# Performance work log

Measured on AMD Instinct MI355X. Metric: run time of the kernel, lower is better.

Reference implementation:

```python
import jax, jax.numpy as jnp
import numpy as np

B, S, H, NH = 4, 384, 256, 8
DH = H // NH


def setup_inputs() -> dict:
    key = jax.random.key(0)
    ks = jax.random.split(key, 16)
    inp = {
        'key': jax.random.normal(ks[0], (B, S, H), jnp.float32),
        'query': jax.random.normal(ks[1], (B, S, H), jnp.float32),
        'value': jax.random.normal(ks[2], (B, S, H), jnp.float32),
        'rel_pos_embedding': jax.random.normal(ks[3], (B, S, S, H), jnp.float32),
        'seq_len': jax.random.randint(ks[4], (B,), 0, 300, jnp.int32),
        'lex_num': jax.random.randint(ks[5], (B,), 0, 84, jnp.int32),
        'Wk': jax.random.normal(ks[6], (H, H), jnp.float32) / np.sqrt(H),
        'bk': jnp.zeros((H,), jnp.float32),
        'Wq': jax.random.normal(ks[7], (H, H), jnp.float32) / np.sqrt(H),
        'bq': jnp.zeros((H,), jnp.float32),
        'Wv': jax.random.normal(ks[8], (H, H), jnp.float32) / np.sqrt(H),
        'bv': jnp.zeros((H,), jnp.float32),
        'Wr': jax.random.normal(ks[9], (H, H), jnp.float32) / np.sqrt(H),
        'br': jnp.zeros((H,), jnp.float32),
    }
    return inp


def reference(key, query, value, rel_pos_embedding, seq_len, lex_num,
              Wk, bk, Wq, bq, Wv, bv, Wr, br):
    b, s, h = key.shape
    # linear projections then split heads: [B, NH, S, DH]
    k = (key @ Wk + bk).reshape(b, s, NH, DH).transpose(0, 2, 1, 3)
    q = (query @ Wq + bq).reshape(b, s, NH, DH).transpose(0, 2, 1, 3)
    v = (value @ Wv + bv).reshape(b, s, NH, DH).transpose(0, 2, 1, 3)
    # relative position projection: [B, Sq, Sk, NH, DH]
    rel = (rel_pos_embedding @ Wr + br).reshape(b, s, s, NH, DH)
    # content term A_C: [B, NH, Sq, Sk]
    A_C = jnp.einsum('bhqd,bhkd->bhqk', q, k)
    # relative term B_D: query dotted with per-(q,k)-pair rel embedding
    B_D = jnp.einsum('bhqd,bqkhd->bhqk', q, rel)
    # key mask from seq_len + lex_num (no scaling by sqrt(d), per original)
    valid = jnp.arange(s)[None, :] < (seq_len + lex_num)[:, None]  # [B, Sk]
    score = jnp.where(valid[:, None, None, :], A_C + B_D, jnp.float32(-1e15))
    attn = jax.nn.softmax(score, axis=-1)
    out = jnp.einsum('bhqk,bhkd->bhqd', attn, v)
    # merge heads: [B, S, H]; note: original does NOT apply w_final
    return out.transpose(0, 2, 1, 3).reshape(b, s, h)
```

## Files before the change

### kernel.cpp

```cpp
#include <hip/hip_runtime.h>
#include <hip/hip_bf16.h>

#define S_  384
#define H_  256
#define NH_ 8
#define DH_ 32
#define B_  4
#define PADK 385

typedef _Float16 f16x8 __attribute__((ext_vector_type(8)));
typedef _Float16 f16x4 __attribute__((ext_vector_type(4)));
typedef float    f32x4 __attribute__((ext_vector_type(4)));

__global__ __launch_bounds__(256) void proj_kernel(
    const float* __restrict__ query, const float* __restrict__ key, const float* __restrict__ value,
    const float* __restrict__ Wq, const float* __restrict__ bq,
    const float* __restrict__ Wk, const float* __restrict__ bk,
    const float* __restrict__ Wv, const float* __restrict__ bv,
    float* __restrict__ Qb, _Float16* __restrict__ Kf, float* __restrict__ Vb)
{
    __shared__ __align__(16) float As[32][36];
    __shared__ __align__(16) float Bs[32][68];
    const int t = threadIdx.x;
    const int m0g = blockIdx.x * 32;
    const int n0g = blockIdx.y * 64;
    const int z = blockIdx.z;
    const float* X    = (z == 0) ? query : (z == 1 ? key : value);
    const float* W    = (z == 0) ? Wq    : (z == 1 ? Wk  : Wv);
    const float* bias = (z == 0) ? bq    : (z == 1 ? bk  : bv);

    const int tn = (t & 15) * 4;
    const int tm = (t >> 4) * 2;
    float acc0[4] = {0.f,0.f,0.f,0.f};
    float acc1[4] = {0.f,0.f,0.f,0.f};

    const int ar = t >> 3, ac4 = (t & 7) * 4;
    const int brr = t >> 4, bc4 = (t & 15) * 4;

    for (int kt = 0; kt < 8; ++kt) {
        const int k0 = kt * 32;
        float4 av  = *(const float4*)&X[(size_t)(m0g + ar) * H_ + k0 + ac4];
        float4 bv0 = *(const float4*)&W[(size_t)(k0 + brr)      * H_ + n0g + bc4];
        float4 bv1 = *(const float4*)&W[(size_t)(k0 + brr + 16) * H_ + n0g + bc4];
        *(float4*)&As[ar][ac4] = av;
        *(float4*)&Bs[brr][bc4] = bv0;
        *(float4*)&Bs[brr + 16][bc4] = bv1;
        __syncthreads();
        #pragma unroll
        for (int c = 0; c < 32; ++c) {
            const float a0 = As[tm][c], a1 = As[tm + 1][c];
            const float4 b4 = *(const float4*)&Bs[c][tn];
            acc0[0] += a0 * b4.x; acc0[1] += a0 * b4.y; acc0[2] += a0 * b4.z; acc0[3] += a0 * b4.w;
            acc1[0] += a1 * b4.x; acc1[1] += a1 * b4.y; acc1[2] += a1 * b4.z; acc1[3] += a1 * b4.w;
        }
        __syncthreads();
    }
    const float4 bi = *(const float4*)&bias[n0g + tn];
    float4 o0 = make_float4(acc0[0] + bi.x, acc0[1] + bi.y, acc0[2] + bi.z, acc0[3] + bi.w);
    float4 o1 = make_float4(acc1[0] + bi.x, acc1[1] + bi.y, acc1[2] + bi.z, acc1[3] + bi.w);
    if (z == 1) {
        f16x4 h0 = { (_Float16)o0.x, (_Float16)o0.y, (_Float16)o0.z, (_Float16)o0.w };
        f16x4 h1 = { (_Float16)o1.x, (_Float16)o1.y, (_Float16)o1.z, (_Float16)o1.w };
        *(f16x4*)&Kf[(size_t)(m0g + tm)     * H_ + n0g + tn] = h0;
        *(f16x4*)&Kf[(size_t)(m0g + tm + 1) * H_ + n0g + tn] = h1;
    } else {
        float* Out = (z == 0) ? Qb : Vb;
        *(float4*)&Out[(size_t)(m0g + tm)     * H_ + n0g + tn] = o0;
        *(float4*)&Out[(size_t)(m0g + tm + 1) * H_ + n0g + tn] = o1;
    }
}

__global__ __launch_bounds__(256) void qw_kernel(
    const float* __restrict__ Qb, const float* __restrict__ Wr,
    _Float16* __restrict__ Af)
{
    __shared__ __align__(16) float Qs[16][36];
    const int t = threadIdx.x;
    const int m0 = blockIdx.x * 16;
    const int h = blockIdx.y;

    float4 wr4[8];
    #pragma unroll
    for (int j = 0; j < 8; ++j)
        wr4[j] = *(const float4*)&Wr[(size_t)t * H_ + h * DH_ + j * 4];

    if (t < 128) {
        const int r = t >> 3, d4 = (t & 7) * 4;
        *(float4*)&Qs[r][d4] = *(const float4*)&Qb[(size_t)(m0 + r) * H_ + h * DH_ + d4];
    }
    __syncthreads();

    const bool own = ((t >> 5) == h);
    #pragma unroll 4
    for (int r = 0; r < 16; ++r) {
        float acc = 0.f;
        #pragma unroll
        for (int j = 0; j < 8; ++j) {
            const float4 qv = *(const float4*)&Qs[r][j * 4];
            acc += qv.x * wr4[j].x + qv.y * wr4[j].y + qv.z * wr4[j].z + qv.w * wr4[j].w;
        }
        _Float16* arow = Af + ((size_t)(m0 + r) * NH_ + h) * 512;
        arow[t] = (_Float16)acc;
        arow[256 + t] = own ? (_Float16)Qs[r][t & 31] : (_Float16)0.0f;
    }
}

__global__ __launch_bounds__(256) void attn_kernel(
    const float* __restrict__ rpe, const _Float16* __restrict__ Af,
    const _Float16* __restrict__ Kf, const float* __restrict__ Vb,
    const int* __restrict__ seq_len, const int* __restrict__ lex_num,
    float* __restrict__ out)
{
    __shared__ float sc[NH_ * PADK];
    __shared__ __align__(16) _Float16 stg[4][16][256];
    const int blk = blockIdx.x;
    const int b = blk / S_;
    const int q = blk - b * S_;
    const int t = threadIdx.x;
    const int lane = t & 63;
    const int wave = t >> 6;
    int limit = seq_len[b] + lex_num[b];
    limit = limit < 0 ? 0 : (limit > S_ ? S_ : limit);
    const size_t rowQ = (size_t)(b * S_ + q);

    if (limit == 0) {
        float acc = 0.f;
        const float* vb = Vb + (size_t)b * S_ * H_ + t;
        for (int k = 0; k < S_; ++k) acc += vb[(size_t)k * H_];
        out[rowQ * H_ + t] = acc * (1.0f / S_);
        return;
    }

    const int r = lane & 15;
    const int g = lane >> 4;

    f16x8 afrag[16];
    {
        const _Float16* Arow = Af + rowQ * (NH_ * 512) + (size_t)r * 512;
        if (r < NH_) {
            #pragma unroll
            for (int j = 0; j < 16; ++j)
                afrag[j] = *(const f16x8*)(Arow + j * 32 + g * 8);
        } else {
            #pragma unroll
            for (int j = 0; j < 16; ++j)
                afrag[j] = (f16x8){};
        }
    }

    char* myl = (char*)&stg[wave][0][0];
    const int swzr = (r & 7) << 4;
    const float* rpe_base = rpe + rowQ * (size_t)S_ * H_;
    const int ntiles = (limit + 15) >> 4;

    for (int kt = wave; kt < ntiles; kt += 4) {
        const int k0 = kt * 16;
        const float* gsrc = rpe_base + (size_t)k0 * H_;
        #pragma unroll
        for (int half = 0; half < 2; ++half) {
            float4 v[8];
            #pragma unroll
            for (int rr = 0; rr < 8; ++rr)
                v[rr] = *(const float4*)&gsrc[(size_t)(half * 8 + rr) * H_ + lane * 4];
            #pragma unroll
            for (int rr = 0; rr < 8; ++rr) {
                const int row = half * 8 + rr;
                f16x4 hv = { (_Float16)v[rr].x, (_Float16)v[rr].y,
                             (_Float16)v[rr].z, (_Float16)v[rr].w };
                *(f16x4*)(myl + row * 512 + ((lane * 8) ^ ((row & 7) << 4))) = hv;
            }
        }
        f32x4 acc = {};
        #pragma unroll
        for (int j = 0; j < 8; ++j) {
            f16x8 bf = *(const f16x8*)(myl + r * 512 + ((j * 64 + g * 16) ^ swzr));
            acc = __builtin_amdgcn_mfma_f32_16x16x32_f16(afrag[j], bf, acc, 0, 0, 0);
        }
        const _Float16* krow = Kf + ((size_t)(b * S_ + k0 + r)) * H_;
        #pragma unroll
        for (int j = 0; j < 8; ++j) {
            f16x8 kf = *(const f16x8*)(krow + j * 32 + g * 8);
            acc = __builtin_amdgcn_mfma_f32_16x16x32_f16(afrag[8 + j], kf, acc, 0, 0, 0);
        }
        if (lane < 32) {
            #pragma unroll
            for (int i = 0; i < 4; ++i)
                sc[(g * 4 + i) * PADK + k0 + r] = acc[i];
        }
    }
    __syncthreads();

    for (int hh = 0; hh < 2; ++hh) {
        const int h = wave * 2 + hh;
        float s0[6];
        #pragma unroll
        for (int j = 0; j < 6; ++j) {
            const int k = lane + 64 * j;
            s0[j] = (k < limit) ? sc[h * PADK + k] : -1e15f;
        }
        float mx = s0[0];
        #pragma unroll
        for (int j = 1; j < 6; ++j) mx = fmaxf(mx, s0[j]);
        #pragma unroll
        for (int m = 1; m < 64; m <<= 1) mx = fmaxf(mx, __shfl_xor(mx, m, 64));
        float p[6]; float sum = 0.f;
        #pragma unroll
        for (int j = 0; j < 6; ++j) {
            const int k = lane + 64 * j;
            p[j] = (k < limit) ? __expf(s0[j] - mx) : 0.f;
            sum += p[j];
        }
        #pragma unroll
        for (int m = 1; m < 64; m <<= 1) sum += __shfl_xor(sum, m, 64);
        const float inv = 1.0f / sum;
        #pragma unroll
        for (int j = 0; j < 6; ++j) sc[h * PADK + lane + 64 * j] = p[j] * inv;
    }
    __syncthreads();

    {
        const int h = t >> 5;
        const int d = t & 31;
        const float* vcol = Vb + (size_t)b * S_ * H_ + h * DH_ + d;
        const float* prow = &sc[h * PADK];
        float acc = 0.f;
        int k = 0;
        for (; k + 8 <= limit; k += 8) {
            float vv[8], pp[8];
            #pragma unroll
            for (int u = 0; u < 8; ++u) vv[u] = vcol[(size_t)(k + u) * H_];
            #pragma unroll
            for (int u = 0; u < 8; ++u) pp[u] = prow[k + u];
            #pragma unroll
            for (int u = 0; u < 8; ++u) acc += pp[u] * vv[u];
        }
        for (; k < limit; ++k) acc += prow[k] * vcol[(size_t)k * H_];
        out[rowQ * H_ + h * DH_ + d] = acc;
    }
}

extern "C" void kernel_launch(void* const* d_in, const int* in_sizes, int n_in,
                              void* d_out, int out_size, void* d_ws, size_t ws_size,
                              hipStream_t stream)
{
    const float* key   = (const float*)d_in[0];
    const float* query = (const float*)d_in[1];
    const float* value = (const float*)d_in[2];
    const float* rpe   = (const float*)d_in[3];
    const int* seq_len = (const int*)d_in[4];
    const int* lex_num = (const int*)d_in[5];
    const float* Wk = (const float*)d_in[6];
    const float* bk = (const float*)d_in[7];
    const float* Wq = (const float*)d_in[8];
    const float* bq = (const float*)d_in[9];
    const float* Wv = (const float*)d_in[10];
    const float* bv = (const float*)d_in[11];
    const float* Wr = (const float*)d_in[12];
    const float* br = (const float*)d_in[13];
    (void)bk; (void)br;

    const size_t NTOK = (size_t)B_ * S_;
    float* w = (float*)d_ws;
    float* Qb = w;
    float* Vb = Qb + NTOK * H_;
    _Float16* Kf = (_Float16*)(Vb + NTOK * H_);
    _Float16* Af = Kf + NTOK * H_;

    proj_kernel<<<dim3(48, 4, 3), dim3(256), 0, stream>>>(
        query, key, value, Wq, bq, Wk, bk, Wv, bv, Qb, Kf, Vb);
    qw_kernel<<<dim3(96, 8), dim3(256), 0, stream>>>(Qb, Wr, Af);
    attn_kernel<<<dim3(1536), dim3(256), 0, stream>>>(
        rpe, Af, Kf, Vb, seq_len, lex_num, (float*)d_out);
}
```

Baseline: 138.2 us.

## Load rpe directly into MFMA B fragments, drop LDS staging and halve A fragments

The attention kernel now reads rel_pos_embedding rows straight from global memory into registers in MFMA B-fragment layout and converts them to fp16 in place, so the per-wave LDS staging buffer and its swizzled stores and reloads go away. The content term uses a Q fragment built on the fly from Qb and selected per row against a zero fragment, so the Af buffer shrinks from 512 to 256 halves per head and the wasted zero rows of afrag are no longer held in registers. Block index mapping interleaves batches (b = blk & 3), and launch bounds request 4 blocks per CU for occupancy. The tradeoff is that each lane's global loads are less coalesced (16 rows strided by H, 32-byte chunks), and the 16 float4 registers per tile raise register pressure.

```diff
diff --git a/kernel.cpp b/kernel.cpp
--- a/kernel.cpp
+++ b/kernel.cpp
@@ -90,7 +90,6 @@
     }
     __syncthreads();
 
-    const bool own = ((t >> 5) == h);
     #pragma unroll 4
     for (int r = 0; r < 16; ++r) {
         float acc = 0.f;
@@ -99,23 +98,21 @@
             const float4 qv = *(const float4*)&Qs[r][j * 4];
             acc += qv.x * wr4[j].x + qv.y * wr4[j].y + qv.z * wr4[j].z + qv.w * wr4[j].w;
         }
-        _Float16* arow = Af + ((size_t)(m0 + r) * NH_ + h) * 512;
-        arow[t] = (_Float16)acc;
-        arow[256 + t] = own ? (_Float16)Qs[r][t & 31] : (_Float16)0.0f;
-    }
-}
-
-__global__ __launch_bounds__(256) void attn_kernel(
+        Af[((size_t)(m0 + r) * NH_ + h) * 256 + t] = (_Float16)acc;
+    }
+}
+
+__global__ __launch_bounds__(256, 4) void attn_kernel(
     const float* __restrict__ rpe, const _Float16* __restrict__ Af,
-    const _Float16* __restrict__ Kf, const float* __restrict__ Vb,
+    const _Float16* __restrict__ Kf, const float* __restrict__ Qb,
+    const float* __restrict__ Vb,
     const int* __restrict__ seq_len, const int* __restrict__ lex_num,
     float* __restrict__ out)
 {
     __shared__ float sc[NH_ * PADK];
-    __shared__ __align__(16) _Float16 stg[4][16][256];
     const int blk = blockIdx.x;
-    const int b = blk / S_;
-    const int q = blk - b * S_;
+    const int b = blk & 3;
+    const int q = blk >> 2;
     const int t = threadIdx.x;
     const int lane = t & 63;
     const int wave = t >> 6;
@@ -133,54 +130,56 @@
 
     const int r = lane & 15;
     const int g = lane >> 4;
-
-    f16x8 afrag[16];
+    const int rc = r & 7;
+
+    f16x8 afrag[8];
     {
-        const _Float16* Arow = Af + rowQ * (NH_ * 512) + (size_t)r * 512;
-        if (r < NH_) {
-            #pragma unroll
-            for (int j = 0; j < 16; ++j)
-                afrag[j] = *(const f16x8*)(Arow + j * 32 + g * 8);
-        } else {
-            #pragma unroll
-            for (int j = 0; j < 16; ++j)
-                afrag[j] = (f16x8){};
-        }
-    }
-
-    char* myl = (char*)&stg[wave][0][0];
-    const int swzr = (r & 7) << 4;
+        const _Float16* Arow = Af + (rowQ * NH_ + rc) * 256 + g * 8;
+        #pragma unroll
+        for (int j = 0; j < 8; ++j)
+            afrag[j] = *(const f16x8*)(Arow + j * 32);
+    }
+    f16x8 qfrag;
+    {
+        const float* qsrc = Qb + rowQ * H_ + rc * 32 + g * 8;
+        const float4 q0 = *(const float4*)qsrc;
+        const float4 q1 = *(const float4*)(qsrc + 4);
+        qfrag[0] = (_Float16)q0.x; qfrag[1] = (_Float16)q0.y;
+        qfrag[2] = (_Float16)q0.z; qfrag[3] = (_Float16)q0.w;
+        qfrag[4] = (_Float16)q1.x; qfrag[5] = (_Float16)q1.y;
+        qfrag[6] = (_Float16)q1.z; qfrag[7] = (_Float16)q1.w;
+    }
+    const f16x8 zfrag = {};
+
     const float* rpe_base = rpe + rowQ * (size_t)S_ * H_;
     const int ntiles = (limit + 15) >> 4;
 
     for (int kt = wave; kt < ntiles; kt += 4) {
         const int k0 = kt * 16;
-        const float* gsrc = rpe_base + (size_t)k0 * H_;
-        #pragma unroll
-        for (int half = 0; half < 2; ++half) {
-            float4 v[8];
-            #pragma unroll
-            for (int rr = 0; rr < 8; ++rr)
-                v[rr] = *(const float4*)&gsrc[(size_t)(half * 8 + rr) * H_ + lane * 4];
-            #pragma unroll
-            for (int rr = 0; rr < 8; ++rr) {
-                const int row = half * 8 + rr;
-                f16x4 hv = { (_Float16)v[rr].x, (_Float16)v[rr].y,
-                             (_Float16)v[rr].z, (_Float16)v[rr].w };
-                *(f16x4*)(myl + row * 512 + ((lane * 8) ^ ((row & 7) << 4))) = hv;
-            }
+        const float* rrow = rpe_base + (size_t)(k0 + r) * H_ + g * 8;
+        float4 rv[16];
+        #pragma unroll
+        for (int j = 0; j < 8; ++j) {
+            rv[2 * j]     = *(const float4*)(rrow + j * 32);
+            rv[2 * j + 1] = *(const float4*)(rrow + j * 32 + 4);
         }
         f32x4 acc = {};
         #pragma unroll
         for (int j = 0; j < 8; ++j) {
-            f16x8 bf = *(const f16x8*)(myl + r * 512 + ((j * 64 + g * 16) ^ swzr));
+            const float4 a = rv[2 * j], c = rv[2 * j + 1];
+            f16x8 bf;
+            bf[0] = (_Float16)a.x; bf[1] = (_Float16)a.y;
+            bf[2] = (_Float16)a.z; bf[3] = (_Float16)a.w;
+            bf[4] = (_Float16)c.x; bf[5] = (_Float16)c.y;
+            bf[6] = (_Float16)c.z; bf[7] = (_Float16)c.w;
             acc = __builtin_amdgcn_mfma_f32_16x16x32_f16(afrag[j], bf, acc, 0, 0, 0);
         }
-        const _Float16* krow = Kf + ((size_t)(b * S_ + k0 + r)) * H_;
-        #pragma unroll
-        for (int j = 0; j < 8; ++j) {
-            f16x8 kf = *(const f16x8*)(krow + j * 32 + g * 8);
-            acc = __builtin_amdgcn_mfma_f32_16x16x32_f16(afrag[8 + j], kf, acc, 0, 0, 0);
+        const _Float16* krow = Kf + ((size_t)(b * S_ + k0 + r)) * H_ + g * 8;
+        #pragma unroll
+        for (int j = 0; j < 8; ++j) {
+            const f16x8 kf = *(const f16x8*)(krow + j * 32);
+            const f16x8 af = (r == j) ? qfrag : zfrag;
+            acc = __builtin_amdgcn_mfma_f32_16x16x32_f16(af, kf, acc, 0, 0, 0);
         }
         if (lane < 32) {
             #pragma unroll
@@ -270,5 +269,5 @@
         query, key, value, Wq, bq, Wk, bk, Wv, bv, Qb, Kf, Vb);
     qw_kernel<<<dim3(96, 8), dim3(256), 0, stream>>>(Qb, Wr, Af);
     attn_kernel<<<dim3(1536), dim3(256), 0, stream>>>(
-        rpe, Af, Kf, Vb, seq_len, lex_num, (float*)d_out);
-}
+        rpe, Af, Kf, Qb, Vb, seq_len, lex_num, (float*)d_out);
+}
```

Result: slower. 187.2 us (+35.4%).

## Stream rel_pos tiles straight to LDS via global_load_lds and convert on read

Applied to the files above, without the earlier changes.

Swaps the register-staged load and fp16 convert of each 16x256 rel_pos_embedding tile for direct global-to-LDS DMA loads (global_load_lds, 16 bytes per lane) into an fp32 staging buffer with a rotated swizzle. The fp16 conversion moves to the MFMA operand read, using packed round-toward-zero converts. The goal is to cut VGPR pressure and the VALU and store instructions on the dominant rpe stream. In exchange it doubles LDS staging space, waits on vmcnt(0) each tile with no prefetch, and changes rounding from round-to-nearest to round-toward-zero.

```diff
diff --git a/kernel.cpp b/kernel.cpp
--- a/kernel.cpp
+++ b/kernel.cpp
@@ -1,5 +1,6 @@
 #include <hip/hip_runtime.h>
 #include <hip/hip_bf16.h>
+#include <stdint.h>
 
 #define S_  384
 #define H_  256
@@ -112,7 +113,7 @@
     float* __restrict__ out)
 {
     __shared__ float sc[NH_ * PADK];
-    __shared__ __align__(16) _Float16 stg[4][16][256];
+    __shared__ __align__(16) float stgf[4][16][256];
     const int blk = blockIdx.x;
     const int b = blk / S_;
     const int q = blk - b * S_;
@@ -148,38 +149,47 @@
         }
     }
 
-    char* myl = (char*)&stg[wave][0][0];
-    const int swzr = (r & 7) << 4;
-    const float* rpe_base = rpe + rowQ * (size_t)S_ * H_;
+    char* myl = (char*)&stgf[wave][0][0];
+    const char* rpe_slab = (const char*)(rpe + rowQ * (size_t)S_ * H_);
     const int ntiles = (limit + 15) >> 4;
+
+    int off[16];
+    #pragma unroll
+    for (int rr = 0; rr < 16; ++rr)
+        off[rr] = (wave * 16 + rr) * 1024 + (((lane & ~7) | ((lane - rr) & 7)) << 4);
+
+    const int c0 = (((g * 2)     + r) & 7) * 16;
+    const int c1 = (((g * 2) + 1 + r) & 7) * 16;
+    const char* mrow = myl + r * 1024;
 
     for (int kt = wave; kt < ntiles; kt += 4) {
         const int k0 = kt * 16;
-        const float* gsrc = rpe_base + (size_t)k0 * H_;
-        #pragma unroll
-        for (int half = 0; half < 2; ++half) {
-            float4 v[8];
-            #pragma unroll
-            for (int rr = 0; rr < 8; ++rr)
-                v[rr] = *(const float4*)&gsrc[(size_t)(half * 8 + rr) * H_ + lane * 4];
-            #pragma unroll
-            for (int rr = 0; rr < 8; ++rr) {
-                const int row = half * 8 + rr;
-                f16x4 hv = { (_Float16)v[rr].x, (_Float16)v[rr].y,
-                             (_Float16)v[rr].z, (_Float16)v[rr].w };
-                *(f16x4*)(myl + row * 512 + ((lane * 8) ^ ((row & 7) << 4))) = hv;
-            }
-        }
+        #pragma unroll
+        for (int rr = 0; rr < 16; ++rr) {
+            __builtin_amdgcn_global_load_lds(
+                (const __attribute__((address_space(1))) uint32_t*)(rpe_slab + off[rr]),
+                (__attribute__((address_space(3))) uint32_t*)(myl + rr * 1024),
+                16, 0, 0);
+            off[rr] += 65536;
+        }
+        asm volatile("s_waitcnt vmcnt(0)" ::: "memory");
+
         f32x4 acc = {};
         #pragma unroll
         for (int j = 0; j < 8; ++j) {
-            f16x8 bf = *(const f16x8*)(myl + r * 512 + ((j * 64 + g * 16) ^ swzr));
-            acc = __builtin_amdgcn_mfma_f32_16x16x32_f16(afrag[j], bf, acc, 0, 0, 0);
-        }
-        const _Float16* krow = Kf + ((size_t)(b * S_ + k0 + r)) * H_;
+            const float4 a  = *(const float4*)(mrow + j * 128 + c0);
+            const float4 a2 = *(const float4*)(mrow + j * 128 + c1);
+            union { decltype(__builtin_amdgcn_cvt_pkrtz(0.f, 0.f)) h2[4]; f16x8 h8; } u;
+            u.h2[0] = __builtin_amdgcn_cvt_pkrtz(a.x,  a.y);
+            u.h2[1] = __builtin_amdgcn_cvt_pkrtz(a.z,  a.w);
+            u.h2[2] = __builtin_amdgcn_cvt_pkrtz(a2.x, a2.y);
+            u.h2[3] = __builtin_amdgcn_cvt_pkrtz(a2.z, a2.w);
+            acc = __builtin_amdgcn_mfma_f32_16x16x32_f16(afrag[j], u.h8, acc, 0, 0, 0);
+        }
+        const _Float16* krow = Kf + ((size_t)(b * S_ + k0 + r)) * H_ + g * 8;
         #pragma unroll
         for (int j = 0; j < 8; ++j) {
-            f16x8 kf = *(const f16x8*)(krow + j * 32 + g * 8);
+            const f16x8 kf = *(const f16x8*)(krow + j * 32);
             acc = __builtin_amdgcn_mfma_f32_16x16x32_f16(afrag[8 + j], kf, acc, 0, 0, 0);
         }
         if (lane < 32) {
```

Result: slower. 148.9 us (+7.7%).

## Store V as transposed fp16 and vectorize the attention-times-V loop

Applied to the files above, without the earlier changes.

The V projection is now written as fp16 in a per-batch transposed [H][S] layout. The PV accumulation can then read contiguous f16x8 vectors of V along the key axis together with float4 probability rows; PADK is raised to 388 so those float4 loads are aligned. The barrier between softmax and PV is dropped, which is safe because each wave only consumes the heads it normalised itself. The cost is extra fp16 rounding on V, plus strided 4-byte scattered stores in the projection epilogue.

```diff
diff --git a/kernel.cpp b/kernel.cpp
--- a/kernel.cpp
+++ b/kernel.cpp
@@ -6,10 +6,11 @@
 #define NH_ 8
 #define DH_ 32
 #define B_  4
-#define PADK 385
+#define PADK 388
 
 typedef _Float16 f16x8 __attribute__((ext_vector_type(8)));
 typedef _Float16 f16x4 __attribute__((ext_vector_type(4)));
+typedef _Float16 f16x2 __attribute__((ext_vector_type(2)));
 typedef float    f32x4 __attribute__((ext_vector_type(4)));
 
 __global__ __launch_bounds__(256) void proj_kernel(
@@ -17,7 +18,7 @@
     const float* __restrict__ Wq, const float* __restrict__ bq,
     const float* __restrict__ Wk, const float* __restrict__ bk,
     const float* __restrict__ Wv, const float* __restrict__ bv,
-    float* __restrict__ Qb, _Float16* __restrict__ Kf, float* __restrict__ Vb)
+    float* __restrict__ Qb, _Float16* __restrict__ Kf, _Float16* __restrict__ Vtf)
 {
     __shared__ __align__(16) float As[32][36];
     __shared__ __align__(16) float Bs[32][68];
@@ -63,10 +64,20 @@
         f16x4 h1 = { (_Float16)o1.x, (_Float16)o1.y, (_Float16)o1.z, (_Float16)o1.w };
         *(f16x4*)&Kf[(size_t)(m0g + tm)     * H_ + n0g + tn] = h0;
         *(f16x4*)&Kf[(size_t)(m0g + tm + 1) * H_ + n0g + tn] = h1;
+    } else if (z == 0) {
+        *(float4*)&Qb[(size_t)(m0g + tm)     * H_ + n0g + tn] = o0;
+        *(float4*)&Qb[(size_t)(m0g + tm + 1) * H_ + n0g + tn] = o1;
     } else {
-        float* Out = (z == 0) ? Qb : Vb;
-        *(float4*)&Out[(size_t)(m0g + tm)     * H_ + n0g + tn] = o0;
-        *(float4*)&Out[(size_t)(m0g + tm + 1) * H_ + n0g + tn] = o1;
+        const int bb = m0g / S_;
+        const int s0 = (m0g - bb * S_) + tm;
+        _Float16* vt = Vtf + (size_t)bb * H_ * S_;
+        const float* p0 = &o0.x;
+        const float* p1 = &o1.x;
+        #pragma unroll
+        for (int j = 0; j < 4; ++j) {
+            f16x2 pair = { (_Float16)p0[j], (_Float16)p1[j] };
+            *(f16x2*)&vt[(size_t)(n0g + tn + j) * S_ + s0] = pair;
+        }
     }
 }
 
@@ -107,7 +118,7 @@
 
 __global__ __launch_bounds__(256) void attn_kernel(
     const float* __restrict__ rpe, const _Float16* __restrict__ Af,
-    const _Float16* __restrict__ Kf, const float* __restrict__ Vb,
+    const _Float16* __restrict__ Kf, const _Float16* __restrict__ Vtf,
     const int* __restrict__ seq_len, const int* __restrict__ lex_num,
     float* __restrict__ out)
 {
@@ -124,9 +135,13 @@
     const size_t rowQ = (size_t)(b * S_ + q);
 
     if (limit == 0) {
+        const _Float16* vrow = Vtf + ((size_t)b * H_ + t) * S_;
         float acc = 0.f;
-        const float* vb = Vb + (size_t)b * S_ * H_ + t;
-        for (int k = 0; k < S_; ++k) acc += vb[(size_t)k * H_];
+        for (int s = 0; s < S_; s += 8) {
+            const f16x8 v8 = *(const f16x8*)(vrow + s);
+            #pragma unroll
+            for (int u = 0; u < 8; ++u) acc += (float)v8[u];
+        }
         out[rowQ * H_ + t] = acc * (1.0f / S_);
         return;
     }
@@ -176,10 +191,10 @@
             f16x8 bf = *(const f16x8*)(myl + r * 512 + ((j * 64 + g * 16) ^ swzr));
             acc = __builtin_amdgcn_mfma_f32_16x16x32_f16(afrag[j], bf, acc, 0, 0, 0);
         }
-        const _Float16* krow = Kf + ((size_t)(b * S_ + k0 + r)) * H_;
+        const _Float16* krow = Kf + ((size_t)(b * S_ + k0 + r)) * H_ + g * 8;
         #pragma unroll
         for (int j = 0; j < 8; ++j) {
-            f16x8 kf = *(const f16x8*)(krow + j * 32 + g * 8);
+            const f16x8 kf = *(const f16x8*)(krow + j * 32);
             acc = __builtin_amdgcn_mfma_f32_16x16x32_f16(afrag[8 + j], kf, acc, 0, 0, 0);
         }
         if (lane < 32) {
@@ -216,25 +231,24 @@
         #pragma unroll
         for (int j = 0; j < 6; ++j) sc[h * PADK + lane + 64 * j] = p[j] * inv;
     }
-    __syncthreads();
 
     {
         const int h = t >> 5;
         const int d = t & 31;
-        const float* vcol = Vb + (size_t)b * S_ * H_ + h * DH_ + d;
+        const _Float16* vrow = Vtf + ((size_t)b * H_ + h * DH_ + d) * S_;
         const float* prow = &sc[h * PADK];
         float acc = 0.f;
         int k = 0;
         for (; k + 8 <= limit; k += 8) {
-            float vv[8], pp[8];
-            #pragma unroll
-            for (int u = 0; u < 8; ++u) vv[u] = vcol[(size_t)(k + u) * H_];
-            #pragma unroll
-            for (int u = 0; u < 8; ++u) pp[u] = prow[k + u];
-            #pragma unroll
-            for (int u = 0; u < 8; ++u) acc += pp[u] * vv[u];
-        }
-        for (; k < limit; ++k) acc += prow[k] * vcol[(size_t)k * H_];
+            const f16x8 v8 = *(const f16x8*)(vrow + k);
+            const float4 p0 = *(const float4*)(prow + k);
+            const float4 p1 = *(const float4*)(prow + k + 4);
+            acc += (float)v8[0] * p0.x + (float)v8[1] * p0.y
+                 + (float)v8[2] * p0.z + (float)v8[3] * p0.w
+                 + (float)v8[4] * p1.x + (float)v8[5] * p1.y
+                 + (float)v8[6] * p1.z + (float)v8[7] * p1.w;
+        }
+        for (; k < limit; ++k) acc += (float)vrow[k] * prow[k];
         out[rowQ * H_ + h * DH_ + d] = acc;
     }
 }
@@ -262,13 +276,13 @@
     const size_t NTOK = (size_t)B_ * S_;
     float* w = (float*)d_ws;
     float* Qb = w;
-    float* Vb = Qb + NTOK * H_;
-    _Float16* Kf = (_Float16*)(Vb + NTOK * H_);
+    _Float16* Kf = (_Float16*)(Qb + NTOK * H_);
     _Float16* Af = Kf + NTOK * H_;
+    _Float16* Vtf = Af + NTOK * NH_ * 512;
 
     proj_kernel<<<dim3(48, 4, 3), dim3(256), 0, stream>>>(
-        query, key, value, Wq, bq, Wk, bk, Wv, bv, Qb, Kf, Vb);
+        query, key, value, Wq, bq, Wk, bk, Wv, bv, Qb, Kf, Vtf);
     qw_kernel<<<dim3(96, 8), dim3(256), 0, stream>>>(Qb, Wr, Af);
     attn_kernel<<<dim3(1536), dim3(256), 0, stream>>>(
-        rpe, Af, Kf, Vb, seq_len, lex_num, (float*)d_out);
-}
+        rpe, Af, Kf, Vtf, seq_len, lex_num, (float*)d_out);
+}
```

New measurement: 172.8 us. +25.0%, slower.
